# Optimization experiments

Measured on AMD Instinct MI355X. Metric: run time of the kernel, lower is better.

Reference implementation:

```python
import jax, jax.numpy as jnp
import numpy as np

B, H, W, C = 2, 64, 64, 512
GROUPS = 32
EPS = 1e-5


def group_norm(x, gamma, beta):
    b, h, w, c = x.shape
    xg = x.reshape(b, h, w, GROUPS, c // GROUPS)
    mu = xg.mean(axis=(1, 2, 4), keepdims=True)
    var = xg.var(axis=(1, 2, 4), keepdims=True)
    xn = ((xg - mu) * jax.lax.rsqrt(var + EPS)).reshape(b, h, w, c)
    return xn * gamma + beta


def setup_inputs() -> dict:
    key = jax.random.key(0)
    ks = jax.random.split(key, 12)
    wscale = 0.02
    inputs = jax.random.normal(ks[0], (B, H, W, C), jnp.float32)
    gamma = jnp.ones((C,), jnp.float32)
    beta = jnp.zeros((C,), jnp.float32)
    Wq = jax.random.normal(ks[1], (C, C), jnp.float32) * wscale
    bq = jnp.zeros((C,), jnp.float32)
    Wk = jax.random.normal(ks[2], (C, C), jnp.float32) * wscale
    bk = jnp.zeros((C,), jnp.float32)
    Wv = jax.random.normal(ks[3], (C, C), jnp.float32) * wscale
    bv = jnp.zeros((C,), jnp.float32)
    Wp = jax.random.normal(ks[4], (C, C), jnp.float32) * wscale
    bp = jnp.zeros((C,), jnp.float32)
    return {"inputs": inputs, "gamma": gamma, "beta": beta,
            "Wq": Wq, "bq": bq, "Wk": Wk, "bk": bk,
            "Wv": Wv, "bv": bv, "Wp": Wp, "bp": bp}


def reference(inputs, gamma, beta, Wq, bq, Wk, bk, Wv, bv, Wp, bp):
    b, h, w, c = inputs.shape
    x = group_norm(inputs, gamma, beta)
    # QKV projections on [b, h, w, c], flatten spatial to sequence hw
    q = (x @ Wq + bq).reshape(b, h * w, c)
    k = (x @ Wk + bk).reshape(b, h * w, c)
    v = (x @ Wv + bv).reshape(b, h * w, c)
    scale = 1.0 / jnp.sqrt(jnp.asarray(c, q.dtype))
    # y[b,i,j] = <q_i, k_j> / sqrt(c); softmax over keys j (last axis, keras default)
    attn = jax.nn.softmax(jnp.einsum('bqc,bkc->bqk', q, k) * scale, axis=-1)
    # out_i = sum_j attn[i,j] * v_j  (matches v @ y^T in the original)
    o = jnp.einsum('bqk,bkc->bqc', attn, v).reshape(b, h, w, c)
    return (o @ Wp + bp) + inputs
```

## Files before the change

### kernel.cpp

```cpp
#include <hip/hip_runtime.h>
#include <hip/hip_bf16.h>
#include <cstddef>


typedef __bf16 bf16;
typedef __attribute__((ext_vector_type(8))) __bf16 bf16x8;
typedef __attribute__((ext_vector_type(4))) __bf16 bf16x4;
typedef __attribute__((ext_vector_type(4))) float f32x4;

#define SEQ   4096
#define CCH   512
#define NBAT  2
#define NOMASK 0x7FFFFFFF
#define SMEM_BYTES 32768
#define PGRID 1024

__device__ __forceinline__ void grid_bar(unsigned* bar, int idx) {
    __syncthreads();
    if (threadIdx.x == 0) {
        __threadfence();
        __hip_atomic_fetch_add(&bar[idx], 1u, __ATOMIC_RELEASE,
                               __HIP_MEMORY_SCOPE_AGENT);
        while (__hip_atomic_load(&bar[idx], __ATOMIC_RELAXED,
                                 __HIP_MEMORY_SCOPE_AGENT) < (unsigned)PGRID)
            __builtin_amdgcn_s_sleep(1);
        __threadfence();
    }
    __syncthreads();
}

__device__ __forceinline__ void prep_unit(
    char* smem, int bid, const float* __restrict__ x,
    const float* __restrict__ Wq, const float* __restrict__ Wk,
    const float* __restrict__ Wv, const float* __restrict__ Wp,
    const float* __restrict__ bq, const float* __restrict__ bk,
    const float* __restrict__ bv,
    float* __restrict__ statsP, bf16* __restrict__ WqkvT,
    bf16* __restrict__ WpT, float* __restrict__ biasQKV) {
    const int tid = threadIdx.x;
    if (bid < 512) {
        float* red = (float*)smem;
        int bg = bid >> 3, c = bid & 7;
        int b = bg >> 5, g = bg & 31;
        const float* base = x + (size_t)b * SEQ * CCH + g * 16;
        float s = 0.f, ss = 0.f;
        for (int i = tid; i < 2048; i += 256) {
            int sp = c * 512 + (i >> 2), q = i & 3;
            float4 v = *(const float4*)(base + (size_t)sp * CCH + q * 4);
            s  += v.x + v.y + v.z + v.w;
            ss += v.x * v.x + v.y * v.y + v.z * v.z + v.w * v.w;
        }
        #pragma unroll
        for (int o = 32; o > 0; o >>= 1) { s += __shfl_down(s, o); ss += __shfl_down(ss, o); }
        int wave = tid >> 6, lane = tid & 63;
        if (lane == 0) { red[wave] = s; red[4 + wave] = ss; }
        __syncthreads();
        if (tid == 0) {
            statsP[bg * 16 + c]     = red[0] + red[1] + red[2] + red[3];
            statsP[bg * 16 + 8 + c] = red[4] + red[5] + red[6] + red[7];
        }
        __syncthreads();
    } else if (bid < 1536) {
        float (*tile)[33] = (float(*)[33])smem;
        int w = bid - 512;
        int z = w >> 8, rest = w & 255;
        int k0 = (rest >> 4) * 32, n0 = (rest & 15) * 32;
        const float* W = (z == 0) ? Wq : (z == 1) ? Wk : (z == 2) ? Wv : Wp;
        int tx = tid & 31, ty = tid >> 5;
        #pragma unroll
        for (int i = ty; i < 32; i += 8)
            tile[i][tx] = W[(size_t)(k0 + i) * CCH + n0 + tx];
        __syncthreads();
        bf16* dst = (z < 3) ? (WqkvT + (size_t)z * CCH * CCH) : WpT;
        #pragma unroll
        for (int i = ty; i < 32; i += 8)
            dst[(size_t)(n0 + i) * CCH + k0 + tx] = (bf16)tile[tx][i];
        __syncthreads();
    } else {
        for (int i = tid; i < 1536; i += 256) {
            float v = (i < 512) ? bq[i] : (i < 1024) ? bk[i - 512] : bv[i - 1024];
            biasQKV[i] = v;
        }
    }
}

__device__ __forceinline__ void gn_table(char* smem, const float* __restrict__ statsP) {
    float* tbl = (float*)smem;
    const int tid = threadIdx.x;
    if (tid < 64) {
        float S = 0.f, SS = 0.f;
        #pragma unroll
        for (int c = 0; c < 8; ++c) { S += statsP[tid * 16 + c]; SS += statsP[tid * 16 + 8 + c]; }
        float mu = S * (1.f / 65536.f);
        float rs = rsqrtf(SS * (1.f / 65536.f) - mu * mu + 1e-5f);
        tbl[tid * 2] = mu; tbl[tid * 2 + 1] = rs;
    }
    __syncthreads();
}

__device__ __forceinline__ void gn_unit(
    char* smem, int w, const float* __restrict__ x,
    const float* __restrict__ gamma, const float* __restrict__ beta,
    bf16* __restrict__ xn) {
    const float* tbl = (const float*)smem;
    size_t idx = (size_t)w * 256 + threadIdx.x;
    int c4 = (int)(idx & 127);
    int b = (int)(idx >> 19);
    int bg = b * 32 + (c4 >> 2);
    float mu = tbl[bg * 2], rs = tbl[bg * 2 + 1];
    float4 v  = ((const float4*)x)[idx];
    float4 gm = ((const float4*)gamma)[c4];
    float4 bt = ((const float4*)beta)[c4];
    bf16x4 o;
    o[0] = (bf16)((v.x - mu) * rs * gm.x + bt.x);
    o[1] = (bf16)((v.y - mu) * rs * gm.y + bt.y);
    o[2] = (bf16)((v.z - mu) * rs * gm.z + bt.z);
    o[3] = (bf16)((v.w - mu) * rs * gm.w + bt.w);
    ((bf16x4*)xn)[idx] = o;
}

__device__ __forceinline__ void vtrans_unit(char* smem,
                                            const bf16* __restrict__ qkv,
                                            bf16* __restrict__ vT,
                                            int b, int s0, int c0) {
    bf16 (*tile)[65] = (bf16(*)[65])smem;
    const int tx = threadIdx.x & 63;
    const int w = threadIdx.x >> 6;
    #pragma unroll
    for (int i = 0; i < 16; ++i) {
        int row = w + i * 4;
        tile[row][tx] = qkv[((size_t)b * SEQ + s0 + row) * 1536 + 1024 + c0 + tx];
    }
    __syncthreads();
    #pragma unroll
    for (int i = 0; i < 16; ++i) {
        int row = w + i * 4;
        vT[((size_t)b * CCH + c0 + row) * SEQ + s0 + tx] = tile[tx][row];
    }
    __syncthreads();
}

template <int EPI, int BN>
__device__ __forceinline__ void gemm2_body(
    char* smem, int bxi, int byi, int bzi,
    const bf16* __restrict__ A, long long aBatch, int lda,
    const bf16* __restrict__ Bt, long long bBatch, int ldb,
    void* __restrict__ Cout, long long cBatch, int ldc,
    int K, int bkmask, float scale,
    const float* __restrict__ bias, const float* __restrict__ resid,
    float* __restrict__ lsum, long long lsumBatch) {
    constexpr int JN = BN / 32;
    bf16* As = (bf16*)smem;
    bf16* Bs = (bf16*)(smem + 16384);
    const int tid = threadIdx.x;
    const int lane = tid & 63;
    const int wave = tid >> 6;

    int zb = bzi, kc = 0;
    if constexpr (EPI == 2) { kc = zb & 1; zb >>= 1; }
    const long long m0 = (long long)bxi * 128;
    const long long n0 = (long long)byi * BN;
    const bf16* Ab = A + (long long)zb * aBatch + (EPI == 2 ? (long long)kc * 2048 : 0);
    const bf16* Bb = Bt + (long long)zb * bBatch + (EPI == 2 ? (long long)kc * 2048 : 0);

    const int wm = (wave & 1) * 64;
    const int wn = (wave >> 1) * (BN / 2);
    const int fm = lane & 15;
    const int q4 = lane >> 4;

    f32x4 acc[4][JN];
    #pragma unroll
    for (int i = 0; i < 4; ++i)
        #pragma unroll
        for (int j = 0; j < JN; ++j)
            acc[i][j] = (f32x4){0.f, 0.f, 0.f, 0.f};

    const int srow = tid >> 3;
    const int schunk = (tid & 7) ^ (srow & 7);

    for (int k0 = 0; k0 < K; k0 += 64) {
        const int kA = k0 + schunk * 8;
        const int kB = (k0 & bkmask) + schunk * 8;
        #pragma unroll
        for (int cb = 0; cb < 4; ++cb) {
            const bf16* g = Ab + (m0 + cb * 32 + srow) * (long long)lda + kA;
            __builtin_amdgcn_global_load_lds((const __attribute__((address_space(1))) void*)g,
                                             (__attribute__((address_space(3))) void*)&As[cb * 2048 + tid * 8], 16, 0, 0);
        }
        #pragma unroll
        for (int cb = 0; cb < BN / 32; ++cb) {
            const bf16* g = Bb + (n0 + cb * 32 + srow) * (long long)ldb + kB;
            __builtin_amdgcn_global_load_lds((const __attribute__((address_space(1))) void*)g,
                                             (__attribute__((address_space(3))) void*)&Bs[cb * 2048 + tid * 8], 16, 0, 0);
        }
        __syncthreads();
        #pragma unroll
        for (int kcc = 0; kcc < 2; ++kcc) {
            bf16x8 fa[4], fb[JN];
            #pragma unroll
            for (int i = 0; i < 4; ++i) {
                const int row = wm + i * 16 + fm;
                const int sw = ((kcc * 4 + q4) ^ (fm & 7)) * 8;
                fa[i] = *(const bf16x8*)&As[row * 64 + sw];
            }
            #pragma unroll
            for (int j = 0; j < JN; ++j) {
                const int row = wn + j * 16 + fm;
                const int sw = ((kcc * 4 + q4) ^ (fm & 7)) * 8;
                fb[j] = *(const bf16x8*)&Bs[row * 64 + sw];
            }
            #pragma unroll
            for (int i = 0; i < 4; ++i)
                #pragma unroll
                for (int j = 0; j < JN; ++j)
                    acc[i][j] = __builtin_amdgcn_mfma_f32_16x16x32_bf16(fa[i], fb[j], acc[i][j], 0, 0, 0);
        }
        __syncthreads();
    }

    float* lrow = (float*)(smem + 1024);
    if constexpr (EPI == 2) {
        float* lscr = (float*)smem;
        const float* lsb = lsum + (long long)zb * lsumBatch + m0;
        const int row = tid & 127, h = tid >> 7;
        float s = 0.f;
        #pragma unroll
        for (int p = 0; p < 32; ++p)
            s += lsb[(long long)(h * 32 + p) * SEQ + row];
        lscr[tid] = s;
        __syncthreads();
        if (tid < 128) lrow[tid] = 1.f / (lscr[tid] + lscr[tid + 128]);
        __syncthreads();
    }

    const int col = lane & 15;
    const int rowb = (lane >> 4) * 4;

    if constexpr (EPI == 1) {
        bf16* Pb = (bf16*)Cout + (long long)zb * cBatch;
        float* lsw = lsum + (long long)zb * lsumBatch
                   + ((long long)byi * 2 + (wave >> 1)) * SEQ;
        #pragma unroll
        for (int i = 0; i < 4; ++i) {
            float rs[4] = {0.f, 0.f, 0.f, 0.f};
            long long mg = m0 + wm + i * 16 + rowb;
            #pragma unroll
            for (int j = 0; j < JN; ++j) {
                long long ng = n0 + wn + j * 16 + col;
                #pragma unroll
                for (int r = 0; r < 4; ++r) {
                    float e = __expf(acc[i][j][r] * scale);
                    rs[r] += e;
                    Pb[(mg + r) * (long long)ldc + ng] = (bf16)e;
                }
            }
            #pragma unroll
            for (int r = 0; r < 4; ++r) {
                rs[r] += __shfl_xor(rs[r], 1);
                rs[r] += __shfl_xor(rs[r], 2);
                rs[r] += __shfl_xor(rs[r], 4);
                rs[r] += __shfl_xor(rs[r], 8);
            }
            if (col == 0) {
                #pragma unroll
                for (int r = 0; r < 4; ++r) lsw[mg + r] = rs[r];
            }
        }
    } else {
        #pragma unroll
        for (int i = 0; i < 4; ++i) {
            #pragma unroll
            for (int j = 0; j < JN; ++j) {
                long long mg = m0 + wm + i * 16 + rowb;
                long long ng = n0 + wn + j * 16 + col;
                #pragma unroll
                for (int r = 0; r < 4; ++r) {
                    float v = acc[i][j][r];
                    long long m = mg + r;
                    if constexpr (EPI == 0) {
                        ((bf16*)Cout)[m * (long long)ldc + ng] = (bf16)(v + bias[ng]);
                    } else if constexpr (EPI == 2) {
                        float inv = lrow[(int)(m - m0)];
                        ((bf16*)Cout)[(long long)zb * cBatch + m * (long long)ldc
                                      + kc * 512 + ng] = (bf16)(v * inv);
                    } else {
                        ((float*)Cout)[m * (long long)ldc + ng] =
                            v + bias[ng] + resid[m * CCH + ng];
                    }
                }
            }
        }
    }
}

struct FusedArgs {
    const float *x, *gamma, *beta, *Wq, *bq, *Wk, *bk, *Wv, *bv, *Wp, *bp;
    float* out;
    float* statsP; float* biasQKV; bf16* WqkvT; bf16* WpT; bf16* xn;
    float* lsum; bf16* qkv; bf16* o2; bf16* vT; bf16* P;
    unsigned* bar;
};

__global__ __launch_bounds__(256, 4) void persistent(FusedArgs a) {
    __shared__ __align__(16) char smem[SMEM_BYTES];
    const int nb = PGRID;
    const float scale = 0.044194173824159216f;

    for (int w = blockIdx.x; w < 1537; w += nb)
        prep_unit(smem, w, a.x, a.Wq, a.Wk, a.Wv, a.Wp, a.bq, a.bk, a.bv,
                  a.statsP, a.WqkvT, a.WpT, a.biasQKV);
    grid_bar(a.bar, 0);

    gn_table(smem, a.statsP);
    for (int w = blockIdx.x; w < 4096; w += nb)
        gn_unit(smem, w, a.x, a.gamma, a.beta, a.xn);
    grid_bar(a.bar, 1);

    for (int w = blockIdx.x; w < 768; w += nb) {
        int l = w >> 3;
        gemm2_body<0, 128>(smem, (w & 7) * 8 + l / 12, l % 12, 0,
                           a.xn, 0, CCH, a.WqkvT, 0, CCH, a.qkv, 0, 1536,
                           CCH, NOMASK, 1.f, a.biasQKV, nullptr, nullptr, 0);
    }
    grid_bar(a.bar, 2);

    for (int w = blockIdx.x; w < 3072; w += nb) {
        if (w < 1024) {
            int b = w >> 9, r = w & 511;
            vtrans_unit(smem, a.qkv, a.vT, b, (r >> 3) * 64, (r & 7) * 64);
        } else {
            int u = w - 1024;
            int bz = u >> 10, r = u & 1023;
            int l = r >> 3;
            gemm2_body<1, 128>(smem, (r & 7) * 4 + (l >> 5), l & 31, bz,
                               a.qkv, (long long)SEQ * 1536, 1536,
                               a.qkv + 512, (long long)SEQ * 1536, 1536,
                               a.P, (long long)SEQ * SEQ, SEQ,
                               CCH, NOMASK, scale, nullptr, nullptr,
                               a.lsum, 64LL * SEQ);
        }
    }
    grid_bar(a.bar, 3);

    for (int w = blockIdx.x; w < 1024; w += nb) {
        int l = w >> 3;
        int S = (w & 7) * 16 + (l >> 3);
        gemm2_body<2, 64>(smem, S & 31, l & 7, S >> 5,
                          a.P, (long long)SEQ * SEQ, SEQ,
                          a.vT, (long long)CCH * SEQ, SEQ,
                          a.o2, (long long)SEQ * 1024, 1024,
                          2048, NOMASK, 1.f, nullptr, nullptr,
                          a.lsum, 64LL * SEQ);
    }
    grid_bar(a.bar, 4);

    for (int w = blockIdx.x; w < 512; w += nb) {
        int l = w >> 3;
        gemm2_body<3, 64>(smem, (w & 7) * 8 + (l >> 3), l & 7, 0,
                          a.o2, 0, 1024, a.WpT, 0, CCH, a.out, 0, CCH,
                          1024, 511, 1.f, a.bp, a.x, nullptr, 0);
    }
}

__global__ __launch_bounds__(256) void k_prep(
    const float* x, const float* Wq, const float* Wk, const float* Wv,
    const float* Wp, const float* bq, const float* bk, const float* bv,
    float* statsP, bf16* WqkvT, bf16* WpT, float* biasQKV) {
    __shared__ __align__(16) char smem[4352];
    prep_unit(smem, blockIdx.x, x, Wq, Wk, Wv, Wp, bq, bk, bv,
              statsP, WqkvT, WpT, biasQKV);
}

__global__ __launch_bounds__(256) void k_gn(
    const float* x, const float* statsP, const float* gamma,
    const float* beta, bf16* xn) {
    __shared__ __align__(16) char smem[512];
    gn_table(smem, statsP);
    gn_unit(smem, blockIdx.x, x, gamma, beta, xn);
}

__global__ __launch_bounds__(256, 2) void k_qkv_m(
    const bf16* xn, const bf16* WqkvT, bf16* qkv, const float* biasQKV) {
    __shared__ __align__(16) char smem[SMEM_BYTES];
    int w = blockIdx.x, l = w >> 3;
    gemm2_body<0, 128>(smem, (w & 7) * 8 + l / 12, l % 12, 0,
                       xn, 0, CCH, WqkvT, 0, CCH, qkv, 0, 1536,
                       CCH, NOMASK, 1.f, biasQKV, nullptr, nullptr, 0);
}

__global__ __launch_bounds__(256, 2) void k_vtrans_m(const bf16* qkv, bf16* vT) {
    __shared__ __align__(16) char smem[8448];
    int w = blockIdx.x, b = w >> 9, r = w & 511;
    vtrans_unit(smem, qkv, vT, b, (r >> 3) * 64, (r & 7) * 64);
}

__global__ __launch_bounds__(256, 2) void k_qk_m(
    const bf16* qkv, bf16* P, float* lsum, float scale) {
    __shared__ __align__(16) char smem[SMEM_BYTES];
    int w = blockIdx.x;
    int bz = w >> 10, r = w & 1023, l = r >> 3;
    gemm2_body<1, 128>(smem, (r & 7) * 4 + (l >> 5), l & 31, bz,
                       qkv, (long long)SEQ * 1536, 1536,
                       qkv + 512, (long long)SEQ * 1536, 1536,
                       P, (long long)SEQ * SEQ, SEQ,
                       CCH, NOMASK, scale, nullptr, nullptr,
                       lsum, 64LL * SEQ);
}

__global__ __launch_bounds__(256, 2) void k_pv_m(
    const bf16* P, const bf16* vT, bf16* o2, float* lsum) {
    __shared__ __align__(16) char smem[SMEM_BYTES];
    int w = blockIdx.x, l = w >> 3;
    int S = (w & 7) * 16 + (l >> 3);
    gemm2_body<2, 64>(smem, S & 31, l & 7, S >> 5,
                      P, (long long)SEQ * SEQ, SEQ,
                      vT, (long long)CCH * SEQ, SEQ,
                      o2, (long long)SEQ * 1024, 1024,
                      2048, NOMASK, 1.f, nullptr, nullptr,
                      lsum, 64LL * SEQ);
}

__global__ __launch_bounds__(256, 2) void k_proj_m(
    const bf16* o2, const bf16* WpT, float* out, const float* bp,
    const float* x) {
    __shared__ __align__(16) char smem[SMEM_BYTES];
    int w = blockIdx.x, l = w >> 3;
    gemm2_body<3, 64>(smem, (w & 7) * 8 + (l >> 3), l & 7, 0,
                      o2, 0, 1024, WpT, 0, CCH, out, 0, CCH,
                      1024, 511, 1.f, bp, x, nullptr, 0);
}

template <int EPI, int BN>
__global__ __launch_bounds__(256, 2) void k_gemm2(
    const bf16* A, long long aBatch, int lda,
    const bf16* Bt, long long bBatch, int ldb,
    void* Cout, long long cBatch, int ldc,
    int K, int bkmask, float scale,
    const float* bias, const float* resid,
    float* lsum, long long lsumBatch) {
    __shared__ __align__(16) char smem[SMEM_BYTES];
    gemm2_body<EPI, BN>(smem, blockIdx.x, blockIdx.y, blockIdx.z,
                        A, aBatch, lda, Bt, bBatch, ldb, Cout, cBatch, ldc,
                        K, bkmask, scale, bias, resid, lsum, lsumBatch);
}

__global__ __launch_bounds__(256, 2) void k_qk_vtrans(
    const bf16* qkv, bf16* vT, bf16* P, float* lsum, float scale,
    int vtBlocks, long long qkBatch, long long pBatch, long long lsumBatch) {
    __shared__ __align__(16) char smem[SMEM_BYTES];
    const int bid = blockIdx.x;
    if (bid < vtBlocks) {
        int b = bid >> 9, r = bid & 511;
        vtrans_unit(smem, qkv, vT, b, (r >> 3) * 64, (r & 7) * 64);
    } else {
        int q = bid - vtBlocks;
        int bz = q >> 10, r = q & 1023;
        gemm2_body<1, 128>(smem, r >> 5, r & 31, bz,
                           qkv, qkBatch, 1536, qkv + 512, qkBatch, 1536,
                           P, pBatch, SEQ, CCH, NOMASK, scale,
                           nullptr, nullptr, lsum, lsumBatch);
    }
}

extern "C" void kernel_launch(void* const* d_in, const int* in_sizes, int n_in,
                              void* d_out, int out_size, void* d_ws, size_t ws_size,
                              hipStream_t stream) {
    const float* x     = (const float*)d_in[0];
    const float* gamma = (const float*)d_in[1];
    const float* beta  = (const float*)d_in[2];
    const float* Wq    = (const float*)d_in[3];
    const float* bq    = (const float*)d_in[4];
    const float* Wk    = (const float*)d_in[5];
    const float* bk    = (const float*)d_in[6];
    const float* Wv    = (const float*)d_in[7];
    const float* bv    = (const float*)d_in[8];
    const float* Wp    = (const float*)d_in[9];
    const float* bp    = (const float*)d_in[10];
    float* out = (float*)d_out;

    constexpr size_t OFF_STATS = 0;
    constexpr size_t OFF_BIAS  = 4096;
    constexpr size_t OFF_BAR   = 10240;
    constexpr size_t OFF_WQKVT = 12288;
    constexpr size_t OFF_WPT   = 1585152;
    constexpr size_t OFF_XN    = 2109440;
    constexpr size_t OFF_LSUM  = OFF_XN;
    constexpr size_t OFF_QKV   = 10498048;
    constexpr size_t OFF_O2    = OFF_QKV;
    constexpr size_t OFF_VT    = 35663872;
    constexpr size_t OFF_P     = 44052480;
    constexpr size_t NEED_FULL = OFF_P + (size_t)NBAT * SEQ * SEQ * 2;

    char* ws = (char*)d_ws;
    float* statsP  = (float*)(ws + OFF_STATS);
    float* biasQKV = (float*)(ws + OFF_BIAS);
    bf16*  WqkvT   = (bf16*)(ws + OFF_WQKVT);
    bf16*  WpT     = (bf16*)(ws + OFF_WPT);
    bf16*  xn      = (bf16*)(ws + OFF_XN);
    float* lsum    = (float*)(ws + OFF_LSUM);
    bf16*  qkv     = (bf16*)(ws + OFF_QKV);
    bf16*  o2      = (bf16*)(ws + OFF_O2);
    bf16*  vT      = (bf16*)(ws + OFF_VT);
    bf16*  P       = (bf16*)(ws + OFF_P);

    const float scale = 0.044194173824159216f;
    const bool full = ws_size >= NEED_FULL;

    if (full) {
        k_prep<<<1537, 256, 0, stream>>>(x, Wq, Wk, Wv, Wp, bq, bk, bv,
                                         statsP, WqkvT, WpT, biasQKV);
        k_gn<<<4096, 256, 0, stream>>>(x, statsP, gamma, beta, xn);
        k_qkv_m<<<768, 256, 0, stream>>>(xn, WqkvT, qkv, biasQKV);
        k_vtrans_m<<<1024, 256, 0, stream>>>(qkv, vT);
        k_qk_m<<<2048, 256, 0, stream>>>(qkv, P, lsum, scale);
        k_pv_m<<<1024, 256, 0, stream>>>(P, vT, o2, lsum);
        k_proj_m<<<512, 256, 0, stream>>>(o2, WpT, out, bp, x);
    } else {
        k_prep<<<1537, 256, 0, stream>>>(x, Wq, Wk, Wv, Wp, bq, bk, bv,
                                         statsP, WqkvT, WpT, biasQKV);
        k_gn<<<4096, 256, 0, stream>>>(x, statsP, gamma, beta, xn);
        k_gemm2<0, 128><<<dim3(64, 12, 1), 256, 0, stream>>>(
            xn, 0, CCH, WqkvT, 0, CCH, qkv, 0, 1536,
            CCH, NOMASK, 1.f, biasQKV, nullptr, nullptr, 0);
        for (int b = 0; b < NBAT; ++b) {
            const bf16* qb = qkv + (long long)b * SEQ * 1536;
            k_qk_vtrans<<<1536, 256, 0, stream>>>(
                qb, vT + (long long)b * CCH * SEQ, P,
                lsum + (long long)b * 64 * SEQ, scale, 512, 0, 0, 0);
            k_gemm2<2, 128><<<dim3(32, 4, 2), 256, 0, stream>>>(
                P, 0, SEQ, vT + (long long)b * CCH * SEQ, 0, SEQ,
                o2 + (long long)b * SEQ * 1024, 0, 1024,
                2048, NOMASK, 1.f, nullptr, nullptr,
                lsum + (long long)b * 64 * SEQ, 0);
        }
        k_gemm2<3, 64><<<dim3(64, 8, 1), 256, 0, stream>>>(
            o2, 0, 1024, WpT, 0, CCH, out, 0, CCH,
            1024, 511, 1.f, bp, x, nullptr, 0);
    }
}
```

Measured before the change: 227.6 us.

## Replace QK^T GEMM with 256x256-tile pipelined kernel using direct global-to-LDS loads

Adds a dedicated QK^T+exp kernel with 512 threads and 256x256 output tiles. It stages operands through global_load_lds into swizzled double-buffered LDS, with explicit waitcnt/barrier software pipelining and setprio around the MFMAs. The kernel writes exp'd P and per-column-block row sums the same way as before. Larger tiles cut redundant operand traffic per output and are meant to raise MFMA utilisation, at the cost of fewer blocks (512) and larger LDS use that lowers occupancy. The unused persistent kernel and grid barrier are also removed.

New measurement: 218.0 us. -4.2%, faster.

```diff
diff --git a/kernel.cpp b/kernel.cpp
--- a/kernel.cpp
+++ b/kernel.cpp
@@ -13,21 +13,6 @@
 #define NBAT  2
 #define NOMASK 0x7FFFFFFF
 #define SMEM_BYTES 32768
-#define PGRID 1024
-
-__device__ __forceinline__ void grid_bar(unsigned* bar, int idx) {
-    __syncthreads();
-    if (threadIdx.x == 0) {
-        __threadfence();
-        __hip_atomic_fetch_add(&bar[idx], 1u, __ATOMIC_RELEASE,
-                               __HIP_MEMORY_SCOPE_AGENT);
-        while (__hip_atomic_load(&bar[idx], __ATOMIC_RELAXED,
-                                 __HIP_MEMORY_SCOPE_AGENT) < (unsigned)PGRID)
-            __builtin_amdgcn_s_sleep(1);
-        __threadfence();
-    }
-    __syncthreads();
-}
 
 __device__ __forceinline__ void prep_unit(
     char* smem, int bid, const float* __restrict__ x,
@@ -293,72 +278,151 @@
     }
 }
 
-struct FusedArgs {
-    const float *x, *gamma, *beta, *Wq, *bq, *Wk, *bk, *Wv, *bv, *Wp, *bp;
-    float* out;
-    float* statsP; float* biasQKV; bf16* WqkvT; bf16* WpT; bf16* xn;
-    float* lsum; bf16* qkv; bf16* o2; bf16* vT; bf16* P;
-    unsigned* bar;
-};
-
-__global__ __launch_bounds__(256, 4) void persistent(FusedArgs a) {
-    __shared__ __align__(16) char smem[SMEM_BYTES];
-    const int nb = PGRID;
-    const float scale = 0.044194173824159216f;
-
-    for (int w = blockIdx.x; w < 1537; w += nb)
-        prep_unit(smem, w, a.x, a.Wq, a.Wk, a.Wv, a.Wp, a.bq, a.bk, a.bv,
-                  a.statsP, a.WqkvT, a.WpT, a.biasQKV);
-    grid_bar(a.bar, 0);
-
-    gn_table(smem, a.statsP);
-    for (int w = blockIdx.x; w < 4096; w += nb)
-        gn_unit(smem, w, a.x, a.gamma, a.beta, a.xn);
-    grid_bar(a.bar, 1);
-
-    for (int w = blockIdx.x; w < 768; w += nb) {
-        int l = w >> 3;
-        gemm2_body<0, 128>(smem, (w & 7) * 8 + l / 12, l % 12, 0,
-                           a.xn, 0, CCH, a.WqkvT, 0, CCH, a.qkv, 0, 1536,
-                           CCH, NOMASK, 1.f, a.biasQKV, nullptr, nullptr, 0);
-    }
-    grid_bar(a.bar, 2);
-
-    for (int w = blockIdx.x; w < 3072; w += nb) {
-        if (w < 1024) {
-            int b = w >> 9, r = w & 511;
-            vtrans_unit(smem, a.qkv, a.vT, b, (r >> 3) * 64, (r & 7) * 64);
-        } else {
-            int u = w - 1024;
-            int bz = u >> 10, r = u & 1023;
-            int l = r >> 3;
-            gemm2_body<1, 128>(smem, (r & 7) * 4 + (l >> 5), l & 31, bz,
-                               a.qkv, (long long)SEQ * 1536, 1536,
-                               a.qkv + 512, (long long)SEQ * 1536, 1536,
-                               a.P, (long long)SEQ * SEQ, SEQ,
-                               CCH, NOMASK, scale, nullptr, nullptr,
-                               a.lsum, 64LL * SEQ);
-        }
-    }
-    grid_bar(a.bar, 3);
-
-    for (int w = blockIdx.x; w < 1024; w += nb) {
-        int l = w >> 3;
-        int S = (w & 7) * 16 + (l >> 3);
-        gemm2_body<2, 64>(smem, S & 31, l & 7, S >> 5,
-                          a.P, (long long)SEQ * SEQ, SEQ,
-                          a.vT, (long long)CCH * SEQ, SEQ,
-                          a.o2, (long long)SEQ * 1024, 1024,
-                          2048, NOMASK, 1.f, nullptr, nullptr,
-                          a.lsum, 64LL * SEQ);
-    }
-    grid_bar(a.bar, 4);
-
-    for (int w = blockIdx.x; w < 512; w += nb) {
-        int l = w >> 3;
-        gemm2_body<3, 64>(smem, (w & 7) * 8 + (l >> 3), l & 7, 0,
-                          a.o2, 0, 1024, a.WpT, 0, CCH, a.out, 0, CCH,
-                          1024, 511, 1.f, a.bp, a.x, nullptr, 0);
+__global__ __launch_bounds__(512, 2) void k_qk256(
+    const bf16* __restrict__ qkv, bf16* __restrict__ P,
+    float* __restrict__ lsum, float scale) {
+    __shared__ __align__(16) bf16 lds[2][2][256 * 64];
+
+    const int tid  = threadIdx.x;
+    const int lane = tid & 63;
+    const int wave = tid >> 6;
+    const int qm = (wave >> 2) & 1;
+    const int qn = wave & 3;
+    const int fm = lane & 15;
+    const int q4 = lane >> 4;
+
+    const int bid = blockIdx.x;
+    const int xcd = bid & 7, l = bid >> 3;
+    const int bz = xcd >> 2, quad = xcd & 3;
+    const int mt = (quad >> 1) * 8 + (l >> 3);
+    const int nt = (quad & 1) * 8 + (l & 7);
+    const long long m0 = (long long)mt * 256;
+    const long long n0 = (long long)nt * 256;
+    const bf16* Aq = qkv + (long long)bz * SEQ * 1536;
+    const bf16* Bk = Aq + 512;
+
+    const int srow = tid >> 3;
+    const int schunk = tid & 7;
+
+    f32x4 acc[4][4][2];
+    #pragma unroll
+    for (int p = 0; p < 4; ++p)
+        #pragma unroll
+        for (int i = 0; i < 4; ++i)
+            #pragma unroll
+            for (int j = 0; j < 2; ++j)
+                acc[p][i][j] = (f32x4){0.f, 0.f, 0.f, 0.f};
+
+    auto STAGE = [&](int h) {
+        const int th = h >> 2, j = h & 3;
+        const int half = j >> 1;
+        const int ab = j & 1;
+        const bf16* src = ab ? Bk : Aq;
+        const long long base0 = ab ? n0 : m0;
+        const int kc = th * 64 + ((schunk ^ (srow & 7)) << 3);
+        bf16* dst = &lds[th & 1][ab][(half * 128) * 64];
+        #pragma unroll
+        for (int c = 0; c < 2; ++c) {
+            const bf16* g = src + (base0 + half * 128 + c * 64 + srow) * 1536 + kc;
+            __builtin_amdgcn_global_load_lds(
+                (const __attribute__((address_space(1))) void*)g,
+                (__attribute__((address_space(3))) void*)&dst[c * 64 * 64 + tid * 8],
+                16, 0, 0);
+        }
+    };
+
+    #pragma unroll
+    for (int h = 0; h < 6; ++h) STAGE(h);
+    asm volatile("s_waitcnt vmcnt(4)" ::: "memory");
+    __builtin_amdgcn_sched_barrier(0);
+    __builtin_amdgcn_s_barrier();
+    __builtin_amdgcn_sched_barrier(0);
+
+    #pragma unroll
+    for (int T = 0; T < 8; ++T) {
+        #pragma unroll
+        for (int p = 0; p < 4; ++p) {
+            const int mh = p >> 1, nh = p & 1, bi = T & 1;
+            bf16x8 fa[4][2], fb[2][2];
+            #pragma unroll
+            for (int i = 0; i < 4; ++i) {
+                const int R = mh * 128 + qm * 64 + i * 16 + fm;
+                #pragma unroll
+                for (int s = 0; s < 2; ++s)
+                    fa[i][s] = *(const bf16x8*)
+                        &lds[bi][0][R * 64 + ((((s << 2) + q4) ^ (fm & 7)) << 3)];
+            }
+            #pragma unroll
+            for (int j = 0; j < 2; ++j) {
+                const int R = nh * 128 + qn * 32 + j * 16 + fm;
+                #pragma unroll
+                for (int s = 0; s < 2; ++s)
+                    fb[j][s] = *(const bf16x8*)
+                        &lds[bi][1][R * 64 + ((((s << 2) + q4) ^ (fm & 7)) << 3)];
+            }
+            const int h = T * 4 + p + 6;
+            if (h < 32) STAGE(h);
+            __builtin_amdgcn_sched_barrier(0);
+            __builtin_amdgcn_s_barrier();
+            asm volatile("s_waitcnt lgkmcnt(0)" ::: "memory");
+            __builtin_amdgcn_sched_barrier(0);
+            __builtin_amdgcn_s_setprio(1);
+            #pragma unroll
+            for (int i = 0; i < 4; ++i)
+                #pragma unroll
+                for (int j = 0; j < 2; ++j)
+                    #pragma unroll
+                    for (int s = 0; s < 2; ++s)
+                        acc[p][i][j] = __builtin_amdgcn_mfma_f32_16x16x32_bf16(
+                            fa[i][s], fb[j][s], acc[p][i][j], 0, 0, 0);
+            __builtin_amdgcn_s_setprio(0);
+            __builtin_amdgcn_sched_barrier(0);
+            if (p == 3 && T < 6)
+                asm volatile("s_waitcnt vmcnt(4)" ::: "memory");
+            else if (p == 3 && T == 6)
+                asm volatile("s_waitcnt vmcnt(0)" ::: "memory");
+            __builtin_amdgcn_sched_barrier(0);
+            __builtin_amdgcn_s_barrier();
+            __builtin_amdgcn_sched_barrier(0);
+        }
+    }
+
+    const int col16 = lane & 15;
+    const int rowb = (lane >> 4) * 4;
+    bf16* Pb = P + (long long)bz * SEQ * SEQ;
+    float* lsw = lsum + (long long)bz * 64 * SEQ + (long long)(nt * 4 + qn) * SEQ;
+    #pragma unroll
+    for (int mh = 0; mh < 2; ++mh) {
+        #pragma unroll
+        for (int i = 0; i < 4; ++i) {
+            float rs[4] = {0.f, 0.f, 0.f, 0.f};
+            const long long mg = m0 + mh * 128 + qm * 64 + i * 16 + rowb;
+            #pragma unroll
+            for (int nh = 0; nh < 2; ++nh) {
+                const int p = mh * 2 + nh;
+                #pragma unroll
+                for (int j = 0; j < 2; ++j) {
+                    const long long ng = n0 + nh * 128 + qn * 32 + j * 16 + col16;
+                    #pragma unroll
+                    for (int r = 0; r < 4; ++r) {
+                        float e = __expf(acc[p][i][j][r] * scale);
+                        rs[r] += e;
+                        Pb[(mg + r) * (long long)SEQ + ng] = (bf16)e;
+                    }
+                }
+            }
+            #pragma unroll
+            for (int r = 0; r < 4; ++r) {
+                rs[r] += __shfl_xor(rs[r], 1);
+                rs[r] += __shfl_xor(rs[r], 2);
+                rs[r] += __shfl_xor(rs[r], 4);
+                rs[r] += __shfl_xor(rs[r], 8);
+            }
+            if (col16 == 0) {
+                #pragma unroll
+                for (int r = 0; r < 4; ++r) lsw[mg + r] = rs[r];
+            }
+        }
     }
 }
 
@@ -392,19 +456,6 @@
     __shared__ __align__(16) char smem[8448];
     int w = blockIdx.x, b = w >> 9, r = w & 511;
     vtrans_unit(smem, qkv, vT, b, (r >> 3) * 64, (r & 7) * 64);
-}
-
-__global__ __launch_bounds__(256, 2) void k_qk_m(
-    const bf16* qkv, bf16* P, float* lsum, float scale) {
-    __shared__ __align__(16) char smem[SMEM_BYTES];
-    int w = blockIdx.x;
-    int bz = w >> 10, r = w & 1023, l = r >> 3;
-    gemm2_body<1, 128>(smem, (r & 7) * 4 + (l >> 5), l & 31, bz,
-                       qkv, (long long)SEQ * 1536, 1536,
-                       qkv + 512, (long long)SEQ * 1536, 1536,
-                       P, (long long)SEQ * SEQ, SEQ,
-                       CCH, NOMASK, scale, nullptr, nullptr,
-                       lsum, 64LL * SEQ);
 }
 
 __global__ __launch_bounds__(256, 2) void k_pv_m(
@@ -480,7 +531,6 @@
 
     constexpr size_t OFF_STATS = 0;
     constexpr size_t OFF_BIAS  = 4096;
-    constexpr size_t OFF_BAR   = 10240;
     constexpr size_t OFF_WQKVT = 12288;
     constexpr size_t OFF_WPT   = 1585152;
     constexpr size_t OFF_XN    = 2109440;
@@ -512,7 +562,7 @@
         k_gn<<<4096, 256, 0, stream>>>(x, statsP, gamma, beta, xn);
         k_qkv_m<<<768, 256, 0, stream>>>(xn, WqkvT, qkv, biasQKV);
         k_vtrans_m<<<1024, 256, 0, stream>>>(qkv, vT);
-        k_qk_m<<<2048, 256, 0, stream>>>(qkv, P, lsum, scale);
+        k_qk256<<<512, 512, 0, stream>>>(qkv, P, lsum, scale);
         k_pv_m<<<1024, 256, 0, stream>>>(P, vT, o2, lsum);
         k_proj_m<<<512, 256, 0, stream>>>(o2, WpT, out, bp, x);
     } else {
```

## Switch to persistent fused kernel with fine-grained dataflow counters between stages

Applied to the files above, without the earlier changes.

The host now launches the single persistent kernel, which was previously unused, after an occupancy check, falling back to the multi-kernel path otherwise. Inside it, some grid-wide barriers are replaced by per-tile counters: QKV GEMM tiles wait only on their GroupNorm rows, the V transpose waits on its QKV rows, and the output projection waits on its PV rows. This is meant to remove launch gaps and barrier idle time. In exchange it relies on all 1024 blocks being co-resident and on spin-waits that could deadlock or contend.

Result: no change. 224.7 us (-1.3%).

```diff
diff --git a/kernel.cpp b/kernel.cpp
--- a/kernel.cpp
+++ b/kernel.cpp
@@ -23,6 +23,25 @@
                                __HIP_MEMORY_SCOPE_AGENT);
         while (__hip_atomic_load(&bar[idx], __ATOMIC_RELAXED,
                                  __HIP_MEMORY_SCOPE_AGENT) < (unsigned)PGRID)
+            __builtin_amdgcn_s_sleep(1);
+        __threadfence();
+    }
+    __syncthreads();
+}
+
+__device__ __forceinline__ void sig(unsigned* c) {
+    __syncthreads();
+    if (threadIdx.x == 0) {
+        __threadfence();
+        __hip_atomic_fetch_add(c, 1u, __ATOMIC_RELEASE,
+                               __HIP_MEMORY_SCOPE_AGENT);
+    }
+}
+
+__device__ __forceinline__ void waitc(unsigned* c, unsigned tgt) {
+    if (threadIdx.x == 0) {
+        while (__hip_atomic_load(c, __ATOMIC_RELAXED,
+                                 __HIP_MEMORY_SCOPE_AGENT) < tgt)
             __builtin_amdgcn_s_sleep(1);
         __threadfence();
     }
@@ -305,6 +324,9 @@
     __shared__ __align__(16) char smem[SMEM_BYTES];
     const int nb = PGRID;
     const float scale = 0.044194173824159216f;
+    unsigned* XN   = a.bar + 16;
+    unsigned* QKVF = a.bar + 80;
+    unsigned* O2F  = a.bar + 144;
 
     for (int w = blockIdx.x; w < 1537; w += nb)
         prep_unit(smem, w, a.x, a.Wq, a.Wk, a.Wv, a.Wp, a.bq, a.bk, a.bv,
@@ -312,51 +334,59 @@
     grid_bar(a.bar, 0);
 
     gn_table(smem, a.statsP);
-    for (int w = blockIdx.x; w < 4096; w += nb)
+    for (int w = blockIdx.x; w < 4096; w += nb) {
         gn_unit(smem, w, a.x, a.gamma, a.beta, a.xn);
+        sig(&XN[w >> 6]);
+    }
+
+    for (int w = blockIdx.x; w < 1792; w += nb) {
+        if (w < 768) {
+            int l = w >> 3;
+            int m = (w & 7) * 8 + l / 12;
+            waitc(&XN[m], 64);
+            gemm2_body<0, 128>(smem, m, l % 12, 0,
+                               a.xn, 0, CCH, a.WqkvT, 0, CCH, a.qkv, 0, 1536,
+                               CCH, NOMASK, 1.f, a.biasQKV, nullptr, nullptr, 0);
+            sig(&QKVF[m]);
+        } else {
+            int u = w - 768;
+            int b = u >> 9, r = u & 511;
+            int s0 = (r >> 3) * 64, c0 = (r & 7) * 64;
+            waitc(&QKVF[b * 32 + (r >> 4)], 12);
+            vtrans_unit(smem, a.qkv, a.vT, b, s0, c0);
+        }
+    }
     grid_bar(a.bar, 1);
 
-    for (int w = blockIdx.x; w < 768; w += nb) {
-        int l = w >> 3;
-        gemm2_body<0, 128>(smem, (w & 7) * 8 + l / 12, l % 12, 0,
-                           a.xn, 0, CCH, a.WqkvT, 0, CCH, a.qkv, 0, 1536,
-                           CCH, NOMASK, 1.f, a.biasQKV, nullptr, nullptr, 0);
+    for (int w = blockIdx.x; w < 2048; w += nb) {
+        int bz = w >> 10, r = w & 1023, l = r >> 3;
+        gemm2_body<1, 128>(smem, (r & 7) * 4 + (l >> 5), l & 31, bz,
+                           a.qkv, (long long)SEQ * 1536, 1536,
+                           a.qkv + 512, (long long)SEQ * 1536, 1536,
+                           a.P, (long long)SEQ * SEQ, SEQ,
+                           CCH, NOMASK, scale, nullptr, nullptr,
+                           a.lsum, 64LL * SEQ);
     }
     grid_bar(a.bar, 2);
-
-    for (int w = blockIdx.x; w < 3072; w += nb) {
-        if (w < 1024) {
-            int b = w >> 9, r = w & 511;
-            vtrans_unit(smem, a.qkv, a.vT, b, (r >> 3) * 64, (r & 7) * 64);
-        } else {
-            int u = w - 1024;
-            int bz = u >> 10, r = u & 1023;
-            int l = r >> 3;
-            gemm2_body<1, 128>(smem, (r & 7) * 4 + (l >> 5), l & 31, bz,
-                               a.qkv, (long long)SEQ * 1536, 1536,
-                               a.qkv + 512, (long long)SEQ * 1536, 1536,
-                               a.P, (long long)SEQ * SEQ, SEQ,
-                               CCH, NOMASK, scale, nullptr, nullptr,
-                               a.lsum, 64LL * SEQ);
-        }
-    }
-    grid_bar(a.bar, 3);
 
     for (int w = blockIdx.x; w < 1024; w += nb) {
         int l = w >> 3;
         int S = (w & 7) * 16 + (l >> 3);
-        gemm2_body<2, 64>(smem, S & 31, l & 7, S >> 5,
+        int mt = S & 31, band = l & 7, bzf = S >> 5;
+        gemm2_body<2, 64>(smem, mt, band, bzf,
                           a.P, (long long)SEQ * SEQ, SEQ,
                           a.vT, (long long)CCH * SEQ, SEQ,
                           a.o2, (long long)SEQ * 1024, 1024,
                           2048, NOMASK, 1.f, nullptr, nullptr,
                           a.lsum, 64LL * SEQ);
-    }
-    grid_bar(a.bar, 4);
+        sig(&O2F[(bzf >> 1) * 32 + mt]);
+    }
 
     for (int w = blockIdx.x; w < 512; w += nb) {
         int l = w >> 3;
-        gemm2_body<3, 64>(smem, (w & 7) * 8 + (l >> 3), l & 7, 0,
+        int m = (w & 7) * 8 + (l >> 3);
+        waitc(&O2F[m], 16);
+        gemm2_body<3, 64>(smem, m, l & 7, 0,
                           a.o2, 0, 1024, a.WpT, 0, CCH, a.out, 0, CCH,
                           1024, 511, 1.f, a.bp, a.x, nullptr, 0);
     }
@@ -494,6 +524,7 @@
     char* ws = (char*)d_ws;
     float* statsP  = (float*)(ws + OFF_STATS);
     float* biasQKV = (float*)(ws + OFF_BIAS);
+    unsigned* bar  = (unsigned*)(ws + OFF_BAR);
     bf16*  WqkvT   = (bf16*)(ws + OFF_WQKVT);
     bf16*  WpT     = (bf16*)(ws + OFF_WPT);
     bf16*  xn      = (bf16*)(ws + OFF_XN);
@@ -506,7 +537,21 @@
     const float scale = 0.044194173824159216f;
     const bool full = ws_size >= NEED_FULL;
 
+    bool usePersist = false;
     if (full) {
+        int occ = 0;
+        hipError_t oe = hipOccupancyMaxActiveBlocksPerMultiprocessor(
+            &occ, (const void*)persistent, 256, 0);
+        usePersist = (oe == hipSuccess && occ >= 4);
+        if (!usePersist) (void)hipGetLastError();
+    }
+
+    if (usePersist) {
+        hipMemsetAsync(ws + OFF_BAR, 0, 2048, stream);
+        FusedArgs a{x, gamma, beta, Wq, bq, Wk, bk, Wv, bv, Wp, bp, out,
+                    statsP, biasQKV, WqkvT, WpT, xn, lsum, qkv, o2, vT, P, bar};
+        persistent<<<PGRID, 256, 0, stream>>>(a);
+    } else if (full) {
         k_prep<<<1537, 256, 0, stream>>>(x, Wq, Wk, Wv, Wp, bq, bk, bv,
                                          statsP, WqkvT, WpT, biasQKV);
         k_gn<<<4096, 256, 0, stream>>>(x, statsP, gamma, beta, xn);
```

## Launch single persistent kernel with grid barriers instead of seven separate kernels

Applied to the files above, without the earlier changes.

Enables the persistent cooperative kernel, which runs all stages in one launch of 1024 blocks separated by atomic grid barriers, provided occupancy reaches 4 blocks per CU. It also rebalances the work so every stage has exactly 1024 units: prep tiles are handled two per block, and the QKV and projection GEMMs use narrower N tiles (96 and 32). The aim is to remove per-kernel launch gaps and tail underutilisation. The cost is that spin barriers make every block wait on the slowest one, smaller tiles give less data reuse, and correctness depends on all 1024 blocks being co-resident.

After: 223.1 us. 1.02x faster.

```diff
diff --git a/kernel.cpp b/kernel.cpp
--- a/kernel.cpp
+++ b/kernel.cpp
@@ -60,26 +60,30 @@
             statsP[bg * 16 + 8 + c] = red[4] + red[5] + red[6] + red[7];
         }
         __syncthreads();
-    } else if (bid < 1536) {
+        if (bid == 0) {
+            for (int i = tid; i < 1536; i += 256) {
+                float v = (i < 512) ? bq[i] : (i < 1024) ? bk[i - 512] : bv[i - 1024];
+                biasQKV[i] = v;
+            }
+        }
+    } else {
         float (*tile)[33] = (float(*)[33])smem;
-        int w = bid - 512;
-        int z = w >> 8, rest = w & 255;
-        int k0 = (rest >> 4) * 32, n0 = (rest & 15) * 32;
-        const float* W = (z == 0) ? Wq : (z == 1) ? Wk : (z == 2) ? Wv : Wp;
-        int tx = tid & 31, ty = tid >> 5;
-        #pragma unroll
-        for (int i = ty; i < 32; i += 8)
-            tile[i][tx] = W[(size_t)(k0 + i) * CCH + n0 + tx];
-        __syncthreads();
-        bf16* dst = (z < 3) ? (WqkvT + (size_t)z * CCH * CCH) : WpT;
-        #pragma unroll
-        for (int i = ty; i < 32; i += 8)
-            dst[(size_t)(n0 + i) * CCH + k0 + tx] = (bf16)tile[tx][i];
-        __syncthreads();
-    } else {
-        for (int i = tid; i < 1536; i += 256) {
-            float v = (i < 512) ? bq[i] : (i < 1024) ? bk[i - 512] : bv[i - 1024];
-            biasQKV[i] = v;
+        #pragma unroll
+        for (int tt = 0; tt < 2; ++tt) {
+            int t = (bid - 512) * 2 + tt;
+            int z = t >> 8, rest = t & 255;
+            int k0 = (rest >> 4) * 32, n0 = (rest & 15) * 32;
+            const float* W = (z == 0) ? Wq : (z == 1) ? Wk : (z == 2) ? Wv : Wp;
+            int tx = tid & 31, ty = tid >> 5;
+            #pragma unroll
+            for (int i = ty; i < 32; i += 8)
+                tile[i][tx] = W[(size_t)(k0 + i) * CCH + n0 + tx];
+            __syncthreads();
+            bf16* dst = (z < 3) ? (WqkvT + (size_t)z * CCH * CCH) : WpT;
+            #pragma unroll
+            for (int i = ty; i < 32; i += 8)
+                dst[(size_t)(n0 + i) * CCH + k0 + tx] = (bf16)tile[tx][i];
+            __syncthreads();
         }
     }
 }
@@ -306,7 +310,7 @@
     const int nb = PGRID;
     const float scale = 0.044194173824159216f;
 
-    for (int w = blockIdx.x; w < 1537; w += nb)
+    for (int w = blockIdx.x; w < 1024; w += nb)
         prep_unit(smem, w, a.x, a.Wq, a.Wk, a.Wv, a.Wp, a.bq, a.bk, a.bv,
                   a.statsP, a.WqkvT, a.WpT, a.biasQKV);
     grid_bar(a.bar, 0);
@@ -316,11 +320,11 @@
         gn_unit(smem, w, a.x, a.gamma, a.beta, a.xn);
     grid_bar(a.bar, 1);
 
-    for (int w = blockIdx.x; w < 768; w += nb) {
+    for (int w = blockIdx.x; w < 1024; w += nb) {
         int l = w >> 3;
-        gemm2_body<0, 128>(smem, (w & 7) * 8 + l / 12, l % 12, 0,
-                           a.xn, 0, CCH, a.WqkvT, 0, CCH, a.qkv, 0, 1536,
-                           CCH, NOMASK, 1.f, a.biasQKV, nullptr, nullptr, 0);
+        gemm2_body<0, 96>(smem, (w & 7) * 8 + (l >> 4), l & 15, 0,
+                          a.xn, 0, CCH, a.WqkvT, 0, CCH, a.qkv, 0, 1536,
+                          CCH, NOMASK, 1.f, a.biasQKV, nullptr, nullptr, 0);
     }
     grid_bar(a.bar, 2);
 
@@ -330,8 +334,7 @@
             vtrans_unit(smem, a.qkv, a.vT, b, (r >> 3) * 64, (r & 7) * 64);
         } else {
             int u = w - 1024;
-            int bz = u >> 10, r = u & 1023;
-            int l = r >> 3;
+            int bz = u >> 10, r = u & 1023, l = r >> 3;
             gemm2_body<1, 128>(smem, (r & 7) * 4 + (l >> 5), l & 31, bz,
                                a.qkv, (long long)SEQ * 1536, 1536,
                                a.qkv + 512, (long long)SEQ * 1536, 1536,
@@ -354,9 +357,9 @@
     }
     grid_bar(a.bar, 4);
 
-    for (int w = blockIdx.x; w < 512; w += nb) {
+    for (int w = blockIdx.x; w < 1024; w += nb) {
         int l = w >> 3;
-        gemm2_body<3, 64>(smem, (w & 7) * 8 + (l >> 3), l & 7, 0,
+        gemm2_body<3, 32>(smem, (w & 7) * 8 + (l >> 4), l & 15, 0,
                           a.o2, 0, 1024, a.WpT, 0, CCH, a.out, 0, CCH,
                           1024, 511, 1.f, a.bp, a.x, nullptr, 0);
     }
@@ -383,9 +386,9 @@
     const bf16* xn, const bf16* WqkvT, bf16* qkv, const float* biasQKV) {
     __shared__ __align__(16) char smem[SMEM_BYTES];
     int w = blockIdx.x, l = w >> 3;
-    gemm2_body<0, 128>(smem, (w & 7) * 8 + l / 12, l % 12, 0,
-                       xn, 0, CCH, WqkvT, 0, CCH, qkv, 0, 1536,
-                       CCH, NOMASK, 1.f, biasQKV, nullptr, nullptr, 0);
+    gemm2_body<0, 96>(smem, (w & 7) * 8 + (l >> 4), l & 15, 0,
+                      xn, 0, CCH, WqkvT, 0, CCH, qkv, 0, 1536,
+                      CCH, NOMASK, 1.f, biasQKV, nullptr, nullptr, 0);
 }
 
 __global__ __launch_bounds__(256, 2) void k_vtrans_m(const bf16* qkv, bf16* vT) {
@@ -425,7 +428,7 @@
     const float* x) {
     __shared__ __align__(16) char smem[SMEM_BYTES];
     int w = blockIdx.x, l = w >> 3;
-    gemm2_body<3, 64>(smem, (w & 7) * 8 + (l >> 3), l & 7, 0,
+    gemm2_body<3, 32>(smem, (w & 7) * 8 + (l >> 4), l & 15, 0,
                       o2, 0, 1024, WpT, 0, CCH, out, 0, CCH,
                       1024, 511, 1.f, bp, x, nullptr, 0);
 }
@@ -494,6 +497,7 @@
     char* ws = (char*)d_ws;
     float* statsP  = (float*)(ws + OFF_STATS);
     float* biasQKV = (float*)(ws + OFF_BIAS);
+    unsigned* bar  = (unsigned*)(ws + OFF_BAR);
     bf16*  WqkvT   = (bf16*)(ws + OFF_WQKVT);
     bf16*  WpT     = (bf16*)(ws + OFF_WPT);
     bf16*  xn      = (bf16*)(ws + OFF_XN);
@@ -506,17 +510,31 @@
     const float scale = 0.044194173824159216f;
     const bool full = ws_size >= NEED_FULL;
 
+    bool usePersist = false;
     if (full) {
-        k_prep<<<1537, 256, 0, stream>>>(x, Wq, Wk, Wv, Wp, bq, bk, bv,
+        int occ = 0;
+        hipError_t oe = hipOccupancyMaxActiveBlocksPerMultiprocessor(
+            &occ, (const void*)persistent, 256, 0);
+        usePersist = (oe == hipSuccess && occ >= 4);
+        if (!usePersist) (void)hipGetLastError();
+    }
+
+    if (usePersist) {
+        hipMemsetAsync(ws + OFF_BAR, 0, 64, stream);
+        FusedArgs a{x, gamma, beta, Wq, bq, Wk, bk, Wv, bv, Wp, bp, out,
+                    statsP, biasQKV, WqkvT, WpT, xn, lsum, qkv, o2, vT, P, bar};
+        persistent<<<PGRID, 256, 0, stream>>>(a);
+    } else if (full) {
+        k_prep<<<1024, 256, 0, stream>>>(x, Wq, Wk, Wv, Wp, bq, bk, bv,
                                          statsP, WqkvT, WpT, biasQKV);
         k_gn<<<4096, 256, 0, stream>>>(x, statsP, gamma, beta, xn);
-        k_qkv_m<<<768, 256, 0, stream>>>(xn, WqkvT, qkv, biasQKV);
+        k_qkv_m<<<1024, 256, 0, stream>>>(xn, WqkvT, qkv, biasQKV);
         k_vtrans_m<<<1024, 256, 0, stream>>>(qkv, vT);
         k_qk_m<<<2048, 256, 0, stream>>>(qkv, P, lsum, scale);
         k_pv_m<<<1024, 256, 0, stream>>>(P, vT, o2, lsum);
-        k_proj_m<<<512, 256, 0, stream>>>(o2, WpT, out, bp, x);
+        k_proj_m<<<1024, 256, 0, stream>>>(o2, WpT, out, bp, x);
     } else {
-        k_prep<<<1537, 256, 0, stream>>>(x, Wq, Wk, Wv, Wp, bq, bk, bv,
+        k_prep<<<1024, 256, 0, stream>>>(x, Wq, Wk, Wv, Wp, bq, bk, bv,
                                          statsP, WqkvT, WpT, biasQKV);
         k_gn<<<4096, 256, 0, stream>>>(x, statsP, gamma, beta, xn);
         k_gemm2<0, 128><<<dim3(64, 12, 1), 256, 0, stream>>>(
```
